# Performance work log

Hardware: AMD Instinct MI355X
Metric: run time of the kernel (lower is better)

The kernel has to match this reference:

```python
import jax, jax.numpy as jnp
import numpy as np

N = 100000      # nodes
D = 64          # raw node feature dim
E = 3200000     # edges
G = 128         # graphs in batch
RANK = 50
OVER = 10       # randomized-SVD oversampling
NPOW = 4        # subspace (power) iterations
ALPHA = 0.85    # pagerank alpha
HID = 32
NCLS = 696
F = 21 * D      # concat of [x] + 4 hop-1 + 16 hop-2 propagated tensors


def setup_inputs() -> dict:
    key = jax.random.key(0)
    ks = jax.random.split(key, 8)
    x = jax.random.normal(ks[0], (N, D), jnp.float32)
    rows = jax.random.randint(ks[1], (E,), 0, N, jnp.int32)
    cols = jax.random.randint(ks[2], (E,), 0, N, jnp.int32)
    graph_ids = jnp.sort(jax.random.randint(ks[3], (N,), 0, G, jnp.int32))
    w = jax.random.normal(ks[4], (F, 64), jnp.float32) / np.float32(np.sqrt(F))
    W1 = jax.random.normal(ks[5], (64, HID), jnp.float32) / np.float32(8.0)
    b1 = jnp.zeros((HID,), jnp.float32)
    W2 = jax.random.normal(ks[6], (HID, NCLS), jnp.float32) / np.float32(np.sqrt(HID))
    return dict(x=x, rows=rows, cols=cols, graph_ids=graph_ids, num_graphs=G,
                w=w, W1=W1, b1=b1, W2=W2)


def _prop_ops(X, rows, cols, deg, n):
    """Apply the 4 sparse operators to X. A[r,c]=1 per edge (rows[k], cols[k])."""
    ax = jax.ops.segment_sum(X[cols], rows, num_segments=n)          # A @ X
    t = ax / jnp.where(deg > 0, deg, 1.0)[:, None]                   # D^{-1} A @ X (transition)
    pr = ALPHA * t + ((1.0 - ALPHA) / n) * ax                        # pagerank-style operator
    dw = ax / (deg + 1e-5)[:, None]                                  # deepwalk: diag(1/(deg+eps)) A
    return [ax, t, pr, dw]


def _propagated(x, rows, cols):
    n = x.shape[0]
    deg = jax.ops.segment_sum(jnp.ones(rows.shape, x.dtype), rows, num_segments=n)
    h1 = _prop_ops(x, rows, cols, deg, n)                            # 4 tensors, hop 1
    h2 = [t2 for t1 in h1 for t2 in _prop_ops(t1, rows, cols, deg, n)]  # 16 tensors, hop 2
    return jnp.concatenate([x] + h1 + h2, axis=-1)                   # [n, 21*D]


def _rsvd(h, rank, key):
    """Deterministic randomized SVD (Halko et al.), QR-stabilized power iterations."""
    k = rank + OVER
    omega = jax.random.normal(key, (h.shape[1], k), h.dtype)
    Q = jnp.linalg.qr(h @ omega)[0]                                  # [n, k]
    for _ in range(NPOW):
        Q = jnp.linalg.qr(h.T @ Q)[0]
        Q = jnp.linalg.qr(h @ Q)[0]
    B = Q.T @ h                                                      # [k, F]
    ub, s, vt = jnp.linalg.svd(B, full_matrices=False)
    return (Q @ ub)[:, :rank], s[:rank], vt[:rank]


def reference(x, rows, cols, graph_ids, num_graphs, w, W1, b1, W2):
    h = _propagated(x, rows, cols)                                   # [n, F]
    u, s, vt = _rsvd(h, RANK, jax.random.key(42))
    us = u * s                                                       # [n, rank]
    term = us @ (vt @ w)                                             # [n, 64]
    hid = jax.nn.leaky_relu(term @ W1 + b1)                          # Dense + leaky_relu
    out_nodes = hid @ W2                                             # [n, num_classes]
    # pooling_adj.T.normalize_right(): each node belongs to exactly one graph,
    # so the column sums are 1 and this is a per-graph segment sum.
    return jax.ops.segment_sum(out_nodes, graph_ids, num_segments=num_graphs)
```

## Files before the change

### kernel.cpp

```cpp
#include <hip/hip_runtime.h>

#define NN   100000
#define DD   64
#define EE   3200000
#define GG   128
#define FF   1344
#define KK   60
#define RK   50
#define HIDN 32
#define NCL  696
#define BSPLIT 128
#define GSL  64
#define PN   40


typedef short short8 __attribute__((ext_vector_type(8)));
typedef float f32x4 __attribute__((ext_vector_type(4)));

__device__ __forceinline__ unsigned short f2bf(float x){
  unsigned u = __float_as_uint(x);
  unsigned r = u + 0x7fffu + ((u>>16)&1u);
  return (unsigned short)(r>>16);
}
__device__ __forceinline__ float bf2f(unsigned short h){
  return __uint_as_float(((unsigned)h)<<16);
}

__device__ __forceinline__ unsigned rotl32(unsigned x, unsigned r){ return (x<<r)|(x>>(32u-r)); }

__device__ __forceinline__ void threefry(unsigned& x0, unsigned& x1){
  const unsigned ks0 = 0u, ks1 = 42u, ks2 = 0x1BD11BDAu ^ 0u ^ 42u;
  unsigned ks[3] = {ks0, ks1, ks2};
  const unsigned rotA[4] = {13u,15u,26u,6u};
  const unsigned rotB[4] = {17u,29u,16u,24u};
  x0 += ks0; x1 += ks1;
  #pragma unroll
  for (int i = 0; i < 5; ++i){
    #pragma unroll
    for (int j = 0; j < 4; ++j){
      unsigned r = (i & 1) ? rotB[j] : rotA[j];
      x0 += x1; x1 = rotl32(x1, r); x1 ^= x0;
    }
    x0 += ks[(i+1)%3]; x1 += ks[(i+2)%3] + (unsigned)(i+1);
  }
}

__device__ __forceinline__ float bits_to_normal(unsigned bits){
  unsigned mant = bits >> 9;
  float f; { unsigned fb = 0x3f800000u | mant; f = __uint_as_float(fb); }
  f -= 1.0f;
  const float lo = -0.99999994f;
  float u = fmaf(f, 2.0f, lo);
  u = fmaxf(lo, u);
  float w = -log1pf(-u*u);
  float p;
  if (w < 5.0f){
    w -= 2.5f;
    p = 2.81022636e-08f;
    p = fmaf(p, w, 3.43273939e-07f);
    p = fmaf(p, w, -3.5233877e-06f);
    p = fmaf(p, w, -4.39150654e-06f);
    p = fmaf(p, w, 0.00021858087f);
    p = fmaf(p, w, -0.00125372503f);
    p = fmaf(p, w, -0.00417768164f);
    p = fmaf(p, w, 0.246640727f);
    p = fmaf(p, w, 1.50140941f);
  } else {
    w = sqrtf(w) - 3.0f;
    p = -0.000200214257f;
    p = fmaf(p, w, 0.000100950558f);
    p = fmaf(p, w, 0.00134934322f);
    p = fmaf(p, w, -0.00367342844f);
    p = fmaf(p, w, 0.00573950773f);
    p = fmaf(p, w, -0.0076224613f);
    p = fmaf(p, w, 0.00943887047f);
    p = fmaf(p, w, 1.00167406f);
    p = fmaf(p, w, 2.83297682f);
  }
  return 1.41421356f * (p * u);
}

__global__ void k_omega(float* __restrict__ om){
  int i = blockIdx.x*blockDim.x + threadIdx.x;
  if (i >= FF*KK) return;
  unsigned x0 = 0u, x1 = (unsigned)i;
  threefry(x0, x1);
  om[i] = bits_to_normal(x0 ^ x1);
}

__global__ void k_count(const int* __restrict__ rows, int* __restrict__ cnt){
  int e = blockIdx.x*blockDim.x + threadIdx.x;
  if (e < EE) atomicAdd(&cnt[rows[e]], 1);
}

__global__ __launch_bounds__(1024) void k_scan1(const int* __restrict__ cnt,
    int* __restrict__ incl, int* __restrict__ bsums){
  __shared__ int buf[1024];
  int i = blockIdx.x*1024 + threadIdx.x;
  int v = (i < NN) ? cnt[i] : 0;
  buf[threadIdx.x] = v; __syncthreads();
  for (int ofs = 1; ofs < 1024; ofs <<= 1){
    int add = (threadIdx.x >= (unsigned)ofs) ? buf[threadIdx.x - ofs] : 0;
    __syncthreads();
    buf[threadIdx.x] += add;
    __syncthreads();
  }
  if (i < NN) incl[i] = buf[threadIdx.x];
  if (threadIdx.x == 1023) bsums[blockIdx.x] = buf[1023];
}

__global__ void k_scan2(int* __restrict__ bsums, int nb){
  if (threadIdx.x == 0){
    int run = 0;
    for (int i = 0; i < nb; ++i){ int v = bsums[i]; bsums[i] = run; run += v; }
  }
}

__global__ void k_scan3(const int* __restrict__ cnt, const int* __restrict__ bsums,
                        int* __restrict__ rowptr){
  int i = blockIdx.x*blockDim.x + threadIdx.x;
  if (i >= NN) return;
  int incl = rowptr[i];
  int ex = incl - cnt[i] + bsums[i >> 10];
  rowptr[i] = ex;
  if (i == NN-1) rowptr[NN] = ex + cnt[i];
}

__global__ void k_scatter(const int* __restrict__ rows, const int* __restrict__ cols,
                          const int* __restrict__ rowptr, int* __restrict__ tmpc,
                          int* __restrict__ csr){
  int e = blockIdx.x*blockDim.x + threadIdx.x;
  if (e >= EE) return;
  int r = rows[e];
  int p = atomicAdd(&tmpc[r], 1);
  csr[rowptr[r] + p] = cols[e];
}

__global__ void k_degr(const int* __restrict__ cnt, float* __restrict__ r1, float* __restrict__ r2){
  int i = blockIdx.x*blockDim.x + threadIdx.x;
  if (i >= NN) return;
  int d = cnt[i];
  float fd = (float)d;
  r1[i] = (d > 0) ? 1.0f/fd : 1.0f;
  r2[i] = 1.0f/(fd + 1e-5f);
}

__global__ void k_xcvt(const float* __restrict__ x,
                       unsigned short* __restrict__ xh, unsigned short* __restrict__ xl){
  int gid = blockIdx.x*blockDim.x + threadIdx.x;
  if (gid >= NN*64) return;
  float v = x[gid];
  unsigned short h = f2bf(v);
  xh[gid] = h;
  xl[gid] = f2bf(v - bf2f(h));
}

__global__ __launch_bounds__(256) void k_hop1(const float* __restrict__ x,
    const int* __restrict__ rp, const int* __restrict__ cc, float* __restrict__ ax,
    unsigned short* __restrict__ axh, unsigned short* __restrict__ axl){
  int n = blockIdx.x*4 + (threadIdx.x >> 6);
  int lane = threadIdx.x & 63;
  if (n >= NN) return;
  int s = rp[n], e = rp[n+1];
  float acc = 0.f;
  int idx = s;
  for (; idx + 8 <= e; idx += 8){
    int c0 = cc[idx], c1 = cc[idx+1], c2 = cc[idx+2], c3 = cc[idx+3];
    int c4 = cc[idx+4], c5 = cc[idx+5], c6 = cc[idx+6], c7 = cc[idx+7];
    float v0 = x[(size_t)c0*64 + lane];
    float v1 = x[(size_t)c1*64 + lane];
    float v2 = x[(size_t)c2*64 + lane];
    float v3 = x[(size_t)c3*64 + lane];
    float v4 = x[(size_t)c4*64 + lane];
    float v5 = x[(size_t)c5*64 + lane];
    float v6 = x[(size_t)c6*64 + lane];
    float v7 = x[(size_t)c7*64 + lane];
    acc += ((v0 + v1) + (v2 + v3)) + ((v4 + v5) + (v6 + v7));
  }
  for (; idx < e; ++idx) acc += x[(size_t)cc[idx]*64 + lane];
  size_t o = (size_t)n*64 + lane;
  ax[o] = acc;
  unsigned short h = f2bf(acc);
  axh[o] = h;
  axl[o] = f2bf(acc - bf2f(h));
}

__global__ __launch_bounds__(256) void k_hop2(const int* __restrict__ rp, const int* __restrict__ cc,
    const float* __restrict__ ax, const float* __restrict__ r1, const float* __restrict__ r2,
    unsigned short* __restrict__ s0h, unsigned short* __restrict__ s0l,
    unsigned short* __restrict__ s1h, unsigned short* __restrict__ s1l,
    unsigned short* __restrict__ s3h, unsigned short* __restrict__ s3l){
  int n = blockIdx.x*4 + (threadIdx.x >> 6);
  int lane = threadIdx.x & 63;
  if (n >= NN) return;
  int s = rp[n], e = rp[n+1];
  float v_s0 = 0.f, v_s1 = 0.f, v_s3 = 0.f;
  int idx = s;
  for (; idx + 8 <= e; idx += 8){
    int c0 = cc[idx], c1 = cc[idx+1], c2 = cc[idx+2], c3 = cc[idx+3];
    int c4 = cc[idx+4], c5 = cc[idx+5], c6 = cc[idx+6], c7 = cc[idx+7];
    float v0 = ax[(size_t)c0*64 + lane], a0 = r1[c0], b0 = r2[c0];
    float v1 = ax[(size_t)c1*64 + lane], a1 = r1[c1], b1 = r2[c1];
    float v2 = ax[(size_t)c2*64 + lane], a2 = r1[c2], b2 = r2[c2];
    float v3 = ax[(size_t)c3*64 + lane], a3 = r1[c3], b3 = r2[c3];
    float v4 = ax[(size_t)c4*64 + lane], a4 = r1[c4], b4 = r2[c4];
    float v5 = ax[(size_t)c5*64 + lane], a5 = r1[c5], b5 = r2[c5];
    float v6 = ax[(size_t)c6*64 + lane], a6 = r1[c6], b6 = r2[c6];
    float v7 = ax[(size_t)c7*64 + lane], a7 = r1[c7], b7 = r2[c7];
    v_s0 += ((v0 + v1) + (v2 + v3)) + ((v4 + v5) + (v6 + v7));
    v_s1 = fmaf(v0,a0,fmaf(v1,a1,fmaf(v2,a2,fmaf(v3,a3,v_s1))));
    v_s1 = fmaf(v4,a4,fmaf(v5,a5,fmaf(v6,a6,fmaf(v7,a7,v_s1))));
    v_s3 = fmaf(v0,b0,fmaf(v1,b1,fmaf(v2,b2,fmaf(v3,b3,v_s3))));
    v_s3 = fmaf(v4,b4,fmaf(v5,b5,fmaf(v6,b6,fmaf(v7,b7,v_s3))));
  }
  for (; idx < e; ++idx){
    int c = cc[idx];
    float v = ax[(size_t)c*64 + lane];
    v_s0 += v;
    v_s1 = fmaf(v, r1[c], v_s1);
    v_s3 = fmaf(v, r2[c], v_s3);
  }
  size_t o = (size_t)n*64 + lane;
  unsigned short h0 = f2bf(v_s0);
  s0h[o] = h0; s0l[o] = f2bf(v_s0 - bf2f(h0));
  unsigned short h1 = f2bf(v_s1);
  s1h[o] = h1; s1l[o] = f2bf(v_s1 - bf2f(h1));
  unsigned short h3 = f2bf(v_s3);
  s3h[o] = h3; s3l[o] = f2bf(v_s3 - bf2f(h3));
}

__global__ void k_beff(const float* __restrict__ B,
                       unsigned short* __restrict__ Beh, unsigned short* __restrict__ Bel){
  int gid = blockIdx.x*blockDim.x + threadIdx.x;
  if (gid >= 20*4096) return;
  int p = gid >> 12;
  int rem = gid & 4095;
  int c = rem >> 6, r = rem & 63;
  int t = p >> 2, j = p & 3;
  float val = 0.f;
  if (c < KK){
    if (t == 0)      val = (j == 0) ? B[(0*64 + r)*60 + c] : 0.f;
    else if (t == 1) val = B[((1+j)*64 + r)*60 + c];
    else if (t == 2) val = B[((5+j)*64 + r)*60 + c] + 1.5e-6f*B[((13+j)*64 + r)*60 + c];
    else if (t == 3) val = B[((9+j)*64 + r)*60 + c] + 0.85f  *B[((13+j)*64 + r)*60 + c];
    else             val = B[((17+j)*64 + r)*60 + c];
  }
  unsigned short h = f2bf(val);
  Beh[gid] = h;
  Bel[gid] = f2bf(val - bf2f(h));
}

__global__ __launch_bounds__(256) void k_beffT(const float* __restrict__ Z,
    const float* __restrict__ Rtot,
    unsigned short* __restrict__ Beh, unsigned short* __restrict__ Bel){
  __shared__ float Br[64][61];
  __shared__ float Rt[60][64];
  int p = blockIdx.x;
  int t2 = p >> 2, j = p & 3;
  int tid = threadIdx.x;
  if (t2 == 0 && j != 0){
    for (int o = tid; o < 4096; o += 256){ Beh[(size_t)p*4096 + o] = 0; Bel[(size_t)p*4096 + o] = 0; }
    return;
  }
  for (int i = tid; i < 3840; i += 256){
    int r = i >> 6, c = i & 63;
    if (c < 60) Rt[r][c] = Rtot[r*60 + c];
  }
  for (int o = tid; o < 64*60; o += 256){
    int r = o / 60, k = o - (o/60)*60;
    float v;
    if (t2 == 0)      v = Z[(0*64 + r)*60 + k];
    else if (t2 == 1) v = Z[((1+j)*64 + r)*60 + k];
    else if (t2 == 2) v = Z[((5+j)*64 + r)*60 + k] + 1.5e-6f*Z[((13+j)*64 + r)*60 + k];
    else if (t2 == 3) v = Z[((9+j)*64 + r)*60 + k] + 0.85f  *Z[((13+j)*64 + r)*60 + k];
    else              v = Z[((17+j)*64 + r)*60 + k];
    Br[r][k] = v;
  }
  __syncthreads();
  for (int o = tid; o < 4096; o += 256){
    int c = o >> 6, r = o & 63;
    float s = 0.f;
    if (c < KK){
      #pragma unroll 10
      for (int kp = 0; kp < 60; ++kp) s = fmaf(Br[r][kp], Rt[kp][c], s);
    }
    unsigned short h = f2bf(s);
    Beh[(size_t)p*4096 + o] = h;
    Bel[(size_t)p*4096 + o] = f2bf(s - bf2f(h));
  }
}

__device__ __forceinline__ void fma44(const float4 a, const float4 b, float (&acc)[4][4]){
  acc[0][0] = fmaf(a.x,b.x,acc[0][0]); acc[0][1] = fmaf(a.x,b.y,acc[0][1]);
  acc[0][2] = fmaf(a.x,b.z,acc[0][2]); acc[0][3] = fmaf(a.x,b.w,acc[0][3]);
  acc[1][0] = fmaf(a.y,b.x,acc[1][0]); acc[1][1] = fmaf(a.y,b.y,acc[1][1]);
  acc[1][2] = fmaf(a.y,b.z,acc[1][2]); acc[1][3] = fmaf(a.y,b.w,acc[1][3]);
  acc[2][0] = fmaf(a.z,b.x,acc[2][0]); acc[2][1] = fmaf(a.z,b.y,acc[2][1]);
  acc[2][2] = fmaf(a.z,b.z,acc[2][2]); acc[2][3] = fmaf(a.z,b.w,acc[2][3]);
  acc[3][0] = fmaf(a.w,b.x,acc[3][0]); acc[3][1] = fmaf(a.w,b.y,acc[3][1]);
  acc[3][2] = fmaf(a.w,b.z,acc[3][2]); acc[3][3] = fmaf(a.w,b.w,acc[3][3]);
}

__global__ __launch_bounds__(256) void k_fwd(
    const unsigned short* __restrict__ xh, const unsigned short* __restrict__ xl,
    const unsigned short* __restrict__ axh, const unsigned short* __restrict__ axl,
    const unsigned short* __restrict__ s0h, const unsigned short* __restrict__ s0l,
    const unsigned short* __restrict__ s1h, const unsigned short* __restrict__ s1l,
    const unsigned short* __restrict__ s3h, const unsigned short* __restrict__ s3l,
    const unsigned short* __restrict__ Beh, const unsigned short* __restrict__ Bel,
    const float* __restrict__ r1, const float* __restrict__ r2,
    float* __restrict__ Y, float* __restrict__ Cpart){
  __shared__ __align__(16) unsigned short AB[4*64*72];
  __shared__ float cS[4][64];
  unsigned short* Ah = AB;
  unsigned short* Al = AB + 64*72;
  unsigned short* Bh = AB + 2*64*72;
  unsigned short* Bl = AB + 3*64*72;
  float* As2 = (float*)AB;
  const unsigned short* Tsh[5] = {xh, axh, s0h, s1h, s3h};
  const unsigned short* Tsl[5] = {xl, axl, s0l, s1l, s3l};
  int n0 = blockIdx.x*64;
  int tid = threadIdx.x;
  int lane = tid & 63, wid = tid >> 6;
  int rowb = (wid & 1)*32, colb = (wid >> 1)*32;
  int l15 = lane & 15, l4 = lane >> 4;

  if (tid < 64){
    int gn = n0 + tid;
    float r1v = 0.f, r2v = 0.f, one = 0.f;
    if (gn < NN){ r1v = r1[gn]; r2v = r2[gn]; one = 1.f; }
    cS[0][tid] = one;
    cS[1][tid] = r1v;
    cS[2][tid] = fmaf(0.85f, r1v, 1.5e-6f*one);
    cS[3][tid] = r2v;
  }

  f32x4 master[2][2] = {};
  int curt = -1;
  for (int plin = 0; plin < 17; ++plin){
    int t  = (plin == 0) ? 0 : (((plin-1) >> 2) + 1);
    int jj = (plin == 0) ? 0 : ((plin-1) & 3);
    int p  = (plin == 0) ? 0 : (plin + 3);
    if (t != curt){
      __syncthreads();
      const unsigned short* Th = Tsh[t];
      const unsigned short* Tl = Tsl[t];
      #pragma unroll
      for (int l = 0; l < 2; ++l){
        int li = tid + l*256;
        int n = li >> 3, f8 = (li & 7)*8;
        int gn = n0 + n;
        uint4 hv = make_uint4(0,0,0,0), lv = make_uint4(0,0,0,0);
        if (gn < NN){
          hv = *(const uint4*)(Th + (size_t)gn*64 + f8);
          lv = *(const uint4*)(Tl + (size_t)gn*64 + f8);
        }
        *(uint4*)(Ah + n*72 + f8) = hv;
        *(uint4*)(Al + n*72 + f8) = lv;
      }
      curt = t;
    }
    __syncthreads();
    #pragma unroll
    for (int l = 0; l < 2; ++l){
      int li = tid + l*256;
      int c = li >> 3, k8 = (li & 7)*8;
      uint4 hv = *(const uint4*)(Beh + (size_t)p*4096 + c*64 + k8);
      uint4 lv = *(const uint4*)(Bel + (size_t)p*4096 + c*64 + k8);
      *(uint4*)(Bh + c*72 + k8) = hv;
      *(uint4*)(Bl + c*72 + k8) = lv;
    }
    __syncthreads();

    float cvv[2][4];
    #pragma unroll
    for (int rg = 0; rg < 2; ++rg)
      #pragma unroll
      for (int r = 0; r < 4; ++r)
        cvv[rg][r] = cS[jj][rowb + rg*16 + l4*4 + r];

    f32x4 part[2][2] = {};
    #pragma unroll
    for (int s = 0; s < 2; ++s){
      int kc = s*32 + l4*8;
      short8 a0h = *(const short8*)(Ah + (rowb      + l15)*72 + kc);
      short8 a1h = *(const short8*)(Ah + (rowb + 16 + l15)*72 + kc);
      short8 a0l = *(const short8*)(Al + (rowb      + l15)*72 + kc);
      short8 a1l = *(const short8*)(Al + (rowb + 16 + l15)*72 + kc);
      #pragma unroll
      for (int cg = 0; cg < 2; ++cg){
        short8 bh = *(const short8*)(Bh + (colb + cg*16 + l15)*72 + kc);
        short8 bl = *(const short8*)(Bl + (colb + cg*16 + l15)*72 + kc);
        part[0][cg] = __builtin_amdgcn_mfma_f32_16x16x32_bf16(a0h, bh, part[0][cg], 0, 0, 0);
        part[0][cg] = __builtin_amdgcn_mfma_f32_16x16x32_bf16(a0h, bl, part[0][cg], 0, 0, 0);
        part[0][cg] = __builtin_amdgcn_mfma_f32_16x16x32_bf16(a0l, bh, part[0][cg], 0, 0, 0);
        part[1][cg] = __builtin_amdgcn_mfma_f32_16x16x32_bf16(a1h, bh, part[1][cg], 0, 0, 0);
        part[1][cg] = __builtin_amdgcn_mfma_f32_16x16x32_bf16(a1h, bl, part[1][cg], 0, 0, 0);
        part[1][cg] = __builtin_amdgcn_mfma_f32_16x16x32_bf16(a1l, bh, part[1][cg], 0, 0, 0);
      }
    }
    #pragma unroll
    for (int rg = 0; rg < 2; ++rg)
      #pragma unroll
      for (int cg = 0; cg < 2; ++cg)
        #pragma unroll
        for (int r = 0; r < 4; ++r)
          master[rg][cg][r] = fmaf(cvv[rg][r], part[rg][cg][r], master[rg][cg][r]);
  }

  #pragma unroll
  for (int rg = 0; rg < 2; ++rg)
    #pragma unroll
    for (int cg = 0; cg < 2; ++cg)
      #pragma unroll
      for (int r = 0; r < 4; ++r){
        int n = rowb + rg*16 + l4*4 + r;
        int c = colb + cg*16 + l15;
        int gn = n0 + n;
        if (gn < NN && c < KK) Y[(size_t)gn*KK + c] = master[rg][cg][r];
      }

  __syncthreads();
  #pragma unroll
  for (int rg = 0; rg < 2; ++rg)
    #pragma unroll
    for (int cg = 0; cg < 2; ++cg)
      #pragma unroll
      for (int r = 0; r < 4; ++r){
        int n = rowb + rg*16 + l4*4 + r;
        int c = colb + cg*16 + l15;
        As2[n*68 + c] = master[rg][cg][r];
      }
  __syncthreads();
  {
    int tx = tid & 15, ty = tid >> 4;
    float g[4][4] = {};
    #pragma unroll 4
    for (int n = 0; n < 64; ++n){
      float4 a = *(const float4*)(As2 + n*68 + tx*4);
      float4 b = *(const float4*)(As2 + n*68 + ty*4);
      fma44(a, b, g);
    }
    float* slab = Cpart + (size_t)(blockIdx.x & (GSL-1))*3600;
    #pragma unroll
    for (int i = 0; i < 4; ++i){
      int r = tx*4 + i;
      #pragma unroll
      for (int j = 0; j < 4; ++j){
        int c = ty*4 + j;
        if (r < KK && c < KK) atomicAdd(&slab[r*KK + c], g[i][j]);
      }
    }
  }
}

__global__ __launch_bounds__(256) void k_bwd(
    const unsigned short* __restrict__ xh, const unsigned short* __restrict__ xl,
    const unsigned short* __restrict__ axh, const unsigned short* __restrict__ axl,
    const unsigned short* __restrict__ s0h, const unsigned short* __restrict__ s0l,
    const unsigned short* __restrict__ s1h, const unsigned short* __restrict__ s1l,
    const unsigned short* __restrict__ s3h, const unsigned short* __restrict__ s3l,
    const float* __restrict__ Qm, const float* __restrict__ r1, const float* __restrict__ r2,
    float* __restrict__ Ppart){
  const unsigned short* Th = (blockIdx.x==0)?xh:(blockIdx.x==1)?axh:(blockIdx.x==2)?s0h:(blockIdx.x==3)?s1h:s3h;
  const unsigned short* Tl = (blockIdx.x==0)?xl:(blockIdx.x==1)?axl:(blockIdx.x==2)?s0l:(blockIdx.x==3)?s1l:s3l;
  const bool isX = (blockIdx.x == 0);
  const int TT = (NN + 31)/32;
  int per = (TT + BSPLIT - 1)/BSPLIT;
  int t0 = blockIdx.y * per;
  int t1 = t0 + per; if (t1 > TT) t1 = TT;

  __shared__ __align__(16) unsigned short Ah[64*PN];
  __shared__ __align__(16) unsigned short Al[64*PN];
  __shared__ __align__(16) unsigned short Bh3[3*64*PN];
  __shared__ __align__(16) unsigned short Bl3[3*64*PN];

  int tid = threadIdx.x;
  int lane = tid & 63, wid = tid >> 6;
  int rowb = (wid & 1)*32, colb = (wid >> 1)*32;
  int l15 = lane & 15, l4 = lane >> 4;

  for (int o = tid; o < 3*64*PN; o += 256){ Bh3[o] = 0; Bl3[o] = 0; }

  f32x4 master[3][2][2] = {};

  for (int tl = t0; tl < t1; ++tl){
    int nb = tl*32;
    __syncthreads();
    {
      int n = tid >> 3, f8 = (tid & 7)*8;
      int gn = nb + n;
      uint4 hv = make_uint4(0,0,0,0), lv = make_uint4(0,0,0,0);
      if (gn < NN){
        hv = *(const uint4*)(Th + (size_t)gn*64 + f8);
        lv = *(const uint4*)(Tl + (size_t)gn*64 + f8);
      }
      const unsigned short* hp = (const unsigned short*)&hv;
      const unsigned short* lp = (const unsigned short*)&lv;
      #pragma unroll
      for (int i = 0; i < 8; ++i){
        Ah[(f8+i)*PN + n] = hp[i];
        Al[(f8+i)*PN + n] = lp[i];
      }
    }
    #pragma unroll
    for (int l = 0; l < 2; ++l){
      int li = tid + l*256;
      if (li < 480){
        int n = li/15, cq = (li - (li/15)*15)*4;
        int gn = nb + n;
        float4 v = make_float4(0.f,0.f,0.f,0.f);
        float cc0 = 0.f, cc1 = 0.f, cc3 = 0.f;
        if (gn < NN){
          v = *(const float4*)(Qm + (size_t)gn*KK + cq);
          cc0 = 1.f;
          cc1 = isX ? 0.f : r1[gn];
          cc3 = isX ? 0.f : r2[gn];
        }
        float vv[4] = {v.x, v.y, v.z, v.w};
        float cc[3] = {cc0, cc1, cc3};
        #pragma unroll
        for (int jj = 0; jj < 3; ++jj){
          #pragma unroll
          for (int i = 0; i < 4; ++i){
            float sv = cc[jj]*vv[i];
            unsigned short h = f2bf(sv);
            Bh3[jj*64*PN + (cq+i)*PN + n] = h;
            Bl3[jj*64*PN + (cq+i)*PN + n] = f2bf(sv - bf2f(h));
          }
        }
      }
    }
    __syncthreads();
    short8 a0h = *(const short8*)(Ah + (rowb      + l15)*PN + l4*8);
    short8 a1h = *(const short8*)(Ah + (rowb + 16 + l15)*PN + l4*8);
    short8 a0l = *(const short8*)(Al + (rowb      + l15)*PN + l4*8);
    short8 a1l = *(const short8*)(Al + (rowb + 16 + l15)*PN + l4*8);
    #pragma unroll
    for (int jj = 0; jj < 3; ++jj){
      #pragma unroll
      for (int cg = 0; cg < 2; ++cg){
        short8 bh = *(const short8*)(Bh3 + jj*64*PN + (colb + cg*16 + l15)*PN + l4*8);
        short8 bl = *(const short8*)(Bl3 + jj*64*PN + (colb + cg*16 + l15)*PN + l4*8);
        master[jj][0][cg] = __builtin_amdgcn_mfma_f32_16x16x32_bf16(a0h, bh, master[jj][0][cg], 0, 0, 0);
        master[jj][0][cg] = __builtin_amdgcn_mfma_f32_16x16x32_bf16(a0h, bl, master[jj][0][cg], 0, 0, 0);
        master[jj][0][cg] = __builtin_amdgcn_mfma_f32_16x16x32_bf16(a0l, bh, master[jj][0][cg], 0, 0, 0);
        master[jj][1][cg] = __builtin_amdgcn_mfma_f32_16x16x32_bf16(a1h, bh, master[jj][1][cg], 0, 0, 0);
        master[jj][1][cg] = __builtin_amdgcn_mfma_f32_16x16x32_bf16(a1h, bl, master[jj][1][cg], 0, 0, 0);
        master[jj][1][cg] = __builtin_amdgcn_mfma_f32_16x16x32_bf16(a1l, bh, master[jj][1][cg], 0, 0, 0);
      }
    }
  }

  float* dst = Ppart + (size_t)blockIdx.y * 76800;
  #pragma unroll
  for (int jj = 0; jj < 3; ++jj){
    int j = (jj == 2) ? 3 : jj;
    #pragma unroll
    for (int rg = 0; rg < 2; ++rg)
      #pragma unroll
      for (int cg = 0; cg < 2; ++cg)
        #pragma unroll
        for (int r = 0; r < 4; ++r){
          int f = rowb + rg*16 + l4*4 + r;
          int kcol = colb + cg*16 + l15;
          if (kcol < KK)
            dst[(size_t)((blockIdx.x*4 + j)*64 + f)*60 + kcol] = master[jj][rg][cg][r];
        }
  }
}

__global__ void k_zasm(const float* __restrict__ Ppart, float* __restrict__ Z){
  int gid = blockIdx.x*blockDim.x + threadIdx.x;
  if (gid >= FF*KK) return;
  int f = gid / 60, k = gid - (gid/60)*60;
  int b = f >> 6, fi = f & 63;
  auto raw = [&](int t, int j)->float{
    size_t e = (size_t)((t*4 + j)*64 + fi)*60 + k;
    float s = 0.f;
    for (int bb = 0; bb < BSPLIT; ++bb) s += Ppart[(size_t)bb*76800 + e];
    return s;
  };
  auto fetch = [&](int t, int j)->float{
    if (j == 2) return 0.85f*raw(t,1) + 1.5e-6f*raw(t,0);
    return raw(t,j);
  };
  float val;
  if (b == 0)      val = raw(0,0);
  else if (b < 5)  val = fetch(1, b-1);
  else if (b < 9)  val = fetch(2, b-5);
  else if (b < 13) val = fetch(3, b-9);
  else if (b < 17) val = 0.85f*fetch(3, b-13) + 1.5e-6f*fetch(2, b-13);
  else             val = fetch(4, b-17);
  Z[gid] = val;
}

__global__ __launch_bounds__(256) void k_syrkp(const float* __restrict__ X, int nrows,
                                               float* __restrict__ Cpart){
  const int TTs = (nrows + 15)/16;
  int per = (TTs + gridDim.x - 1)/gridDim.x;
  int t0 = blockIdx.x*per;
  int t1 = t0 + per; if (t1 > TTs) t1 = TTs;
  __shared__ float Xs[16][64];
  int tid = threadIdx.x;
  int tx = tid & 15, ty = tid >> 4;
  float acc[4][4] = {};
  for (int tl = t0; tl < t1; ++tl){
    int nbase = tl*16;
    if (tid < 240){
      int n = tid / 15, ci = tid - (tid/15)*15;
      float4 v = make_float4(0.f,0.f,0.f,0.f);
      int gn = nbase + n;
      if (gn < nrows) v = *(const float4*)(X + (size_t)gn*KK + ci*4);
      *(float4*)&Xs[n][ci*4] = v;
    } else {
      int n = tid - 240;
      Xs[n][60]=0.f; Xs[n][61]=0.f; Xs[n][62]=0.f; Xs[n][63]=0.f;
    }
    __syncthreads();
    #pragma unroll
    for (int n = 0; n < 16; ++n){
      float4 a = *(const float4*)&Xs[n][tx*4];
      float4 b = *(const float4*)&Xs[n][ty*4];
      fma44(a, b, acc);
    }
    __syncthreads();
  }
  float* dst = Cpart + (size_t)blockIdx.x*3600;
  #pragma unroll
  for (int i = 0; i < 4; ++i){
    int r = tx*4 + i;
    #pragma unroll
    for (int j = 0; j < 4; ++j){
      int c = ty*4 + j;
      if (r < KK && c < KK) dst[r*KK + c] = acc[i][j];
    }
  }
}

__global__ void k_cred(const float* __restrict__ Cpart, int nparts, float* __restrict__ Cm){
  int gid = blockIdx.x*blockDim.x + threadIdx.x;
  if (gid >= 3600) return;
  float s = 0.f;
  for (int b = 0; b < nparts; ++b) s += Cpart[(size_t)b*3600 + gid];
  Cm[gid] = s;
}

__global__ __launch_bounds__(256) void k_cholinv(const float* __restrict__ Cin,
                                                 float* __restrict__ Rinv){
  __shared__ float R[60][65];
  __shared__ float Ri[60][65];
  __shared__ float Tmp[30][33];
  __shared__ float ridge;
  int t = threadIdx.x;
  for (int i = t; i < 3840; i += 256){
    int r = i >> 6, c = i & 63;
    if (c < 60) R[r][c] = Cin[r*60 + c];
  }
  __syncthreads();
  if (t == 0){
    float tr = 0.f;
    for (int i = 0; i < 60; ++i) tr += R[i][i];
    ridge = 1e-7f*(tr/60.f) + 1e-30f;
  }
  __syncthreads();
  if (t < 60) R[t][t] += ridge;
  __syncthreads();
  for (int j = 0; j < 60; ++j){
    float d  = fmaxf(R[j][j], 1e-30f);
    float dp = (j > 0) ? fmaxf(R[j-1][j-1], 1e-30f) : 1.f;
    float inv = 1.0f / d;
    float rsp = (j > 0) ? (1.0f / sqrtf(dp)) : 1.f;
    int nrow = 59 - j;
    for (int task = t; task < (nrow+1)*64; task += 256){
      int rr = task >> 6, i2 = task & 63;
      if (rr < nrow){
        int k = j + 1 + rr;
        if (i2 >= k && i2 < 60) R[k][i2] -= R[j][k]*R[j][i2]*inv;
      } else {
        if (j > 0 && i2 >= j-1 && i2 < 60) R[j-1][i2] *= rsp;
      }
    }
    __syncthreads();
  }
  if (t == 0) R[59][59] = sqrtf(fmaxf(R[59][59], 1e-30f));
  __syncthreads();
  for (int i = t; i < 3840; i += 256){ int r = i >> 6, c = i & 63; Ri[r][c] = 0.f; }
  __syncthreads();
  if (t < 60){
    int c = t;
    int lo = (c < 30) ? 0 : 30;
    Ri[c][c] = 1.0f / R[c][c];
    for (int i = c-1; i >= lo; --i){
      float s = 0.f;
      for (int k = i+1; k <= c; ++k) s += R[i][k]*Ri[k][c];
      Ri[i][c] = -s / R[i][i];
    }
  }
  __syncthreads();
  for (int idx2 = t; idx2 < 960; idx2 += 256){
    int r = idx2 >> 5, c = idx2 & 31;
    if (c < 30){
      float s = 0.f;
      for (int k = 0; k <= c; ++k) s += R[r][30+k]*Ri[30+k][30+c];
      Tmp[r][c] = s;
    }
  }
  __syncthreads();
  for (int idx2 = t; idx2 < 960; idx2 += 256){
    int r = idx2 >> 5, c = idx2 & 31;
    if (c < 30){
      float s = 0.f;
      for (int k = r; k < 30; ++k) s += Ri[r][k]*Tmp[k][c];
      Ri[r][30+c] = -s;
    }
  }
  __syncthreads();
  for (int i = t; i < 3600; i += 256) Rinv[i] = Ri[i/60][i%60];
}

__global__ __launch_bounds__(256) void k_cholinv2(const float* __restrict__ Gin,
                                                  float* __restrict__ Rinv){
  __shared__ float G[60][65];
  __shared__ float RN[60][65];
  __shared__ float T1[60][65];
  __shared__ float G2[60][65];
  __shared__ float Tmp[30][33];
  __shared__ float ridge;
  int t = threadIdx.x;
  for (int i = t; i < 3840; i += 256){
    int r = i >> 6, c = i & 63;
    if (c < 60){ G[r][c] = Gin[r*60 + c]; RN[r][c] = Rinv[r*60 + c]; }
  }
  __syncthreads();
  for (int o = t; o < 3600; o += 256){
    int i = o/60, j = o - (o/60)*60;
    float s = 0.f;
    for (int k = 0; k <= j; ++k) s = fmaf(G[i][k], RN[k][j], s);
    T1[i][j] = s;
  }
  __syncthreads();
  for (int o = t; o < 3600; o += 256){
    int i = o/60, j = o - (o/60)*60;
    float s = 0.f;
    for (int k = 0; k <= i; ++k) s = fmaf(RN[k][i], T1[k][j], s);
    G2[i][j] = s;
  }
  __syncthreads();
  if (t == 0){
    float tr = 0.f;
    for (int i = 0; i < 60; ++i) tr += G2[i][i];
    ridge = 1e-7f*(tr/60.f) + 1e-30f;
  }
  __syncthreads();
  if (t < 60) G2[t][t] += ridge;
  __syncthreads();
  for (int j = 0; j < 60; ++j){
    float d  = fmaxf(G2[j][j], 1e-30f);
    float dp = (j > 0) ? fmaxf(G2[j-1][j-1], 1e-30f) : 1.f;
    float inv = 1.0f / d;
    float rsp = (j > 0) ? (1.0f / sqrtf(dp)) : 1.f;
    int nrow = 59 - j;
    for (int task = t; task < (nrow+1)*64; task += 256){
      int rr = task >> 6, i2 = task & 63;
      if (rr < nrow){
        int k = j + 1 + rr;
        if (i2 >= k && i2 < 60) G2[k][i2] -= G2[j][k]*G2[j][i2]*inv;
      } else {
        if (j > 0 && i2 >= j-1 && i2 < 60) G2[j-1][i2] *= rsp;
      }
    }
    __syncthreads();
  }
  if (t == 0) G2[59][59] = sqrtf(fmaxf(G2[59][59], 1e-30f));
  __syncthreads();
  for (int i = t; i < 3840; i += 256){ int r = i >> 6, c = i & 63; T1[r][c] = 0.f; }
  __syncthreads();
  if (t < 60){
    int c = t;
    int lo = (c < 30) ? 0 : 30;
    T1[c][c] = 1.0f / G2[c][c];
    for (int i = c-1; i >= lo; --i){
      float s = 0.f;
      for (int k = i+1; k <= c; ++k) s += G2[i][k]*T1[k][c];
      T1[i][c] = -s / G2[i][i];
    }
  }
  __syncthreads();
  for (int idx2 = t; idx2 < 960; idx2 += 256){
    int r = idx2 >> 5, c = idx2 & 31;
    if (c < 30){
      float s = 0.f;
      for (int k = 0; k <= c; ++k) s += G2[r][30+k]*T1[30+k][30+c];
      Tmp[r][c] = s;
    }
  }
  __syncthreads();
  for (int idx2 = t; idx2 < 960; idx2 += 256){
    int r = idx2 >> 5, c = idx2 & 31;
    if (c < 30){
      float s = 0.f;
      for (int k = r; k < 30; ++k) s += T1[r][k]*Tmp[k][c];
      T1[r][30+c] = -s;
    }
  }
  __syncthreads();
  for (int o = t; o < 3600; o += 256){
    int i = o/60, j = o - (o/60)*60;
    float s = 0.f;
    if (i <= j){
      for (int k = i; k <= j; ++k) s = fmaf(RN[i][k], T1[k][j], s);
    }
    Rinv[o] = s;
  }
}

__global__ __launch_bounds__(256) void k_applyR(const float* Yin,
    const float* __restrict__ Rinv, float* Xout, int nrows){
  __shared__ float Rs[3600];
  for (int i = threadIdx.x; i < 3600; i += 256) Rs[i] = Rinv[i];
  __syncthreads();
  int w = threadIdx.x >> 6, lane = threadIdx.x & 63;
  #pragma unroll
  for (int r = 0; r < 4; ++r){
    int n = blockIdx.x*16 + w*4 + r;
    if (n >= nrows) continue;
    const float* y = Yin + (size_t)n*KK;
    float accv = 0.f;
    #pragma unroll 10
    for (int k2 = 0; k2 < KK; ++k2) accv = fmaf(y[k2], Rs[k2*KK + lane], accv);
    if (lane < KK) Xout[(size_t)n*KK + lane] = accv;
  }
}

__global__ void k_wb(const float* __restrict__ Z, const float* __restrict__ w,
                     float* __restrict__ WB){
  int gid = blockIdx.x*blockDim.x + threadIdx.x;
  if (gid >= KK*64) return;
  int r = gid >> 6, d = gid & 63;
  float acc = 0.f;
  for (int f = 0; f < FF; ++f) acc = fmaf(Z[(size_t)f*KK + r], w[(size_t)f*64 + d], acc);
  WB[gid] = acc;
}

__global__ __launch_bounds__(512) void k_jacobi(const float* __restrict__ Min,
                                                float* __restrict__ U50){
  __shared__ float A[60][65];
  __shared__ float Vv[60][65];
  __shared__ float cs[32], sn[32];
  __shared__ int pp[32], qq[32];
  __shared__ float ev[64];
  __shared__ int idx[64];
  int t = threadIdx.x;
  for (int i = t; i < 3840; i += 512){
    int r = i >> 6, c = i & 63;
    if (c < 60){ A[r][c] = Min[r*60 + c]; Vv[r][c] = (r == c) ? 1.f : 0.f; }
  }
  __syncthreads();
  for (int sweep = 0; sweep < 3; ++sweep){
    for (int round = 0; round < 59; ++round){
      if (t < 30){
        int i = t, j2 = 59 - t;
        int p = (i == 0) ? 0 : ((i - 1 + round) % 59 + 1);
        int q = ((j2 - 1 + round) % 59 + 1);
        if (p > q){ int tv = p; p = q; q = tv; }
        pp[t] = p; qq[t] = q;
        float app = A[p][p], aqq = A[q][q], apq = A[p][q];
        float c, s;
        if (fabsf(apq) < 1e-36f){ c = 1.f; s = 0.f; }
        else {
          float tau = (aqq - app) / (2.f * apq);
          float tt = ((tau >= 0.f) ? 1.f : -1.f) / (fabsf(tau) + sqrtf(1.f + tau*tau));
          c = 1.f / sqrtf(1.f + tt*tt);
          s = tt * c;
        }
        cs[t] = c; sn[t] = s;
      }
      __syncthreads();
      for (int task = t; task < 1920; task += 512){
        int k = task >> 6, i = task & 63;
        if (i < 60){
          int p = pp[k], q = qq[k];
          float c = cs[k], s = sn[k];
          float aip = A[i][p], aiq = A[i][q];
          A[i][p] = c*aip - s*aiq;  A[i][q] = s*aip + c*aiq;
          float vip = Vv[i][p], viq = Vv[i][q];
          Vv[i][p] = c*vip - s*viq; Vv[i][q] = s*vip + c*viq;
        }
      }
      __syncthreads();
      for (int task = t; task < 1920; task += 512){
        int k = task >> 6, i = task & 63;
        if (i < 60){
          int p = pp[k], q = qq[k];
          float c = cs[k], s = sn[k];
          float api = A[p][i], aqi = A[q][i];
          A[p][i] = c*api - s*aqi;  A[q][i] = s*api + c*aqi;
        }
      }
      __syncthreads();
    }
  }
  if (t < 60) ev[t] = A[t][t];
  __syncthreads();
  if (t < 60){
    float mine = ev[t];
    int rank = 0;
    for (int j = 0; j < 60; ++j){
      float o = ev[j];
      if (o > mine || (o == mine && j < t)) ++rank;
    }
    if (rank < RK) idx[rank] = t;
  }
  __syncthreads();
  for (int i2 = t; i2 < 60*RK; i2 += 512){
    int r = i2 / RK, c = i2 - (i2/RK)*RK;
    U50[i2] = Vv[r][idx[c]];
  }
}

__global__ __launch_bounds__(256) void k_chain(const float* __restrict__ U50,
    const float* __restrict__ WB, const float* __restrict__ W1, float* __restrict__ TW1){
  __shared__ float Us[60][52];
  __shared__ float WBs[60][64];
  __shared__ float G[50][64];
  __shared__ float Ts[60][64];
  int t = threadIdx.x;
  for (int i = t; i < 60*RK; i += 256) Us[i/RK][i%RK] = U50[i];
  for (int i = t; i < 3840; i += 256) WBs[i>>6][i&63] = WB[i];
  __syncthreads();
  for (int o = t; o < RK*64; o += 256){
    int r = o >> 6, d = o & 63;
    float acc = 0.f;
    #pragma unroll 10
    for (int i = 0; i < KK; ++i) acc = fmaf(Us[i][r], WBs[i][d], acc);
    G[r][d] = acc;
  }
  __syncthreads();
  for (int o = t; o < KK*64; o += 256){
    int i = o >> 6, d = o & 63;
    float acc = 0.f;
    #pragma unroll 10
    for (int r = 0; r < RK; ++r) acc = fmaf(Us[i][r], G[r][d], acc);
    Ts[i][d] = acc;
  }
  __syncthreads();
  for (int o = t; o < KK*HIDN; o += 256){
    int i = o >> 5, j = o & 31;
    float acc = 0.f;
    #pragma unroll 8
    for (int d = 0; d < 64; ++d) acc = fmaf(Ts[i][d], W1[d*HIDN + j], acc);
    TW1[o] = acc;
  }
}

__global__ __launch_bounds__(256) void k_hid(const float* __restrict__ Q,
    const float* __restrict__ TW1, const float* __restrict__ b1, float* __restrict__ hid){
  __shared__ float Ts[KK*HIDN];
  __shared__ float bs[HIDN];
  for (int i = threadIdx.x; i < KK*HIDN; i += 256) Ts[i] = TW1[i];
  if (threadIdx.x < HIDN) bs[threadIdx.x] = b1[threadIdx.x];
  __syncthreads();
  int gid = blockIdx.x*256 + threadIdx.x;
  if (gid >= NN*HIDN) return;
  int n = gid >> 5, j = gid & 31;
  const float* q = Q + (size_t)n*KK;
  float a = bs[j];
  #pragma unroll 10
  for (int k2 = 0; k2 < KK; ++k2) a = fmaf(q[k2], Ts[k2*HIDN + j], a);
  hid[gid] = (a >= 0.f) ? a : 0.01f*a;
}

__global__ void k_gstart(const int* __restrict__ gids, int* __restrict__ gst){
  int g = blockIdx.x*blockDim.x + threadIdx.x;
  if (g > GG) return;
  if (g == GG){ gst[GG] = NN; return; }
  int lo = 0, hi = NN;
  while (lo < hi){ int mid = (lo + hi) >> 1; if (gids[mid] < g) lo = mid + 1; else hi = mid; }
  gst[g] = lo;
}

__global__ __launch_bounds__(256) void k_gpool(const float* __restrict__ hid,
    const int* __restrict__ gst, float* __restrict__ pooled){
  int g = blockIdx.x;
  __shared__ float part[8][32];
  int w = threadIdx.x >> 5, lane = threadIdx.x & 31;
  int s = gst[g], e = gst[g+1];
  float acc = 0.f;
  for (int n = s + w; n < e; n += 8)
    acc += hid[(size_t)n*HIDN + lane];
  part[w][lane] = acc;
  __syncthreads();
  if (w == 0){
    float v = 0.f;
    #pragma unroll
    for (int i = 0; i < 8; ++i) v += part[i][lane];
    pooled[g*HIDN + lane] = v;
  }
}

__global__ void k_out(const float* __restrict__ pooled, const float* __restrict__ W2,
                      float* __restrict__ out){
  int gid = blockIdx.x*blockDim.x + threadIdx.x;
  if (gid >= GG*NCL) return;
  int g = gid / NCL, c = gid - (gid/NCL)*NCL;
  const float* p = pooled + g*HIDN;
  float acc = 0.f;
  #pragma unroll
  for (int k = 0; k < HIDN; ++k) acc = fmaf(p[k], W2[(size_t)k*NCL + c], acc);
  out[gid] = acc;
}

extern "C" void kernel_launch(void* const* d_in, const int* in_sizes, int n_in,
                              void* d_out, int out_size, void* d_ws, size_t ws_size,
                              hipStream_t stream){
  (void)in_sizes; (void)n_in; (void)out_size;
  const float* x   = (const float*)d_in[0];
  const int*  rows = (const int*)d_in[1];
  const int*  cols = (const int*)d_in[2];
  const int*  gids = (const int*)d_in[3];
  const float* wM  = (const float*)d_in[5];
  const float* W1  = (const float*)d_in[6];
  const float* b1  = (const float*)d_in[7];
  const float* W2  = (const float*)d_in[8];
  float* out = (float*)d_out;

  char* base = (char*)d_ws;
  size_t off = 0;
  auto alloc = [&](size_t bytes)->char*{
    off = (off + 255) & ~(size_t)255;
    char* p = base + off; off += bytes; return p;
  };
  float* ax    = (float*)alloc((size_t)NN*64*4);
  unsigned short* xh  = (unsigned short*)alloc((size_t)NN*64*2);
  unsigned short* xl  = (unsigned short*)alloc((size_t)NN*64*2);
  unsigned short* axh = (unsigned short*)alloc((size_t)NN*64*2);
  unsigned short* axl = (unsigned short*)alloc((size_t)NN*64*2);
  unsigned short* s0h = (unsigned short*)alloc((size_t)NN*64*2);
  unsigned short* s0l = (unsigned short*)alloc((size_t)NN*64*2);
  unsigned short* s1h = (unsigned short*)alloc((size_t)NN*64*2);
  unsigned short* s1l = (unsigned short*)alloc((size_t)NN*64*2);
  unsigned short* s3h = (unsigned short*)alloc((size_t)NN*64*2);
  unsigned short* s3l = (unsigned short*)alloc((size_t)NN*64*2);
  float* Y     = (float*)alloc((size_t)NN*KK*4);
  int*   csr   = (int*)  alloc((size_t)EE*4);
  float* Ppart = (float*)alloc((size_t)BSPLIT*76800*4);
  unsigned short* Beh = (unsigned short*)alloc((size_t)20*4096*2);
  unsigned short* Bel = (unsigned short*)alloc((size_t)20*4096*2);
  float* Om    = (float*)alloc((size_t)FF*KK*4);
  float* Zf    = (float*)alloc((size_t)FF*KK*4);
  float* Cm    = (float*)alloc(3600*4);
  float* Rinv  = (float*)alloc(3600*4);
  float* Mm    = (float*)alloc(3600*4);
  float* U50   = (float*)alloc(60*RK*4);
  float* WB    = (float*)alloc(KK*64*4);
  float* TW1   = (float*)alloc(KK*HIDN*4);
  float* pooled= (float*)alloc((size_t)GG*HIDN*4);
  float* r1    = (float*)alloc((size_t)NN*4);
  float* r2    = (float*)alloc((size_t)NN*4);
  int* cnt     = (int*)alloc((size_t)NN*4);
  int* rowptr  = (int*)alloc((size_t)(NN+1)*4);
  int* tmpc    = (int*)alloc((size_t)NN*4);
  int* gst     = (int*)alloc((size_t)(GG+1)*4);
  int* bsums   = (int*)alloc(256*4);
  float* hid   = ax;
  float* Cpart = Ppart;
  if (off > ws_size) return;

  const int SCAN_B = (NN + 1023) / 1024;

  hipMemsetAsync(cnt, 0, (size_t)NN*4, stream);
  k_count<<<(EE+255)/256, 256, 0, stream>>>(rows, cnt);
  k_scan1<<<SCAN_B, 1024, 0, stream>>>(cnt, rowptr, bsums);
  k_scan2<<<1, 64, 0, stream>>>(bsums, SCAN_B);
  k_scan3<<<(NN+255)/256, 256, 0, stream>>>(cnt, bsums, rowptr);
  hipMemsetAsync(tmpc, 0, (size_t)NN*4, stream);
  k_scatter<<<(EE+255)/256, 256, 0, stream>>>(rows, cols, rowptr, tmpc, csr);
  k_degr<<<(NN+255)/256, 256, 0, stream>>>(cnt, r1, r2);

  k_xcvt<<<(NN*64+255)/256, 256, 0, stream>>>(x, xh, xl);
  k_hop1<<<(NN+3)/4, 256, 0, stream>>>(x, rowptr, csr, ax, axh, axl);
  k_hop2<<<(NN+3)/4, 256, 0, stream>>>(rowptr, csr, ax, r1, r2, s0h, s0l, s1h, s1l, s3h, s3l);

  k_omega<<<(FF*KK+255)/256, 256, 0, stream>>>(Om);

  auto fwdg = [&](){
    hipMemsetAsync(Cpart, 0, (size_t)GSL*3600*4, stream);
    k_fwd<<<(NN+63)/64, 256, 0, stream>>>(xh, xl, axh, axl, s0h, s0l, s1h, s1l, s3h, s3l,
                                          Beh, Bel, r1, r2, Y, Cpart);
  };
  auto bwd = [&](const float* Qbuf){
    k_bwd<<<dim3(5, BSPLIT), 256, 0, stream>>>(xh, xl, axh, axl, s0h, s0l, s1h, s1l, s3h, s3l,
                                               Qbuf, r1, r2, Ppart);
    k_zasm<<<(FF*KK+255)/256, 256, 0, stream>>>(Ppart, Zf);
  };

  k_beff<<<(20*4096+255)/256, 256, 0, stream>>>(Om, Beh, Bel);
  fwdg();

  for (int it = 0; it < 4; ++it){
    k_cred<<<15, 256, 0, stream>>>(Cpart, GSL, Cm);
    k_cholinv<<<1, 256, 0, stream>>>(Cm, Rinv);
    bwd(Y);
    k_syrkp<<<84, 256, 0, stream>>>(Zf, FF, Cpart);
    k_cred<<<15, 256, 0, stream>>>(Cpart, 84, Cm);
    k_cholinv2<<<1, 256, 0, stream>>>(Cm, Rinv);
    k_beffT<<<20, 256, 0, stream>>>(Zf, Rinv, Beh, Bel);
    fwdg();
  }

  k_cred<<<15, 256, 0, stream>>>(Cpart, GSL, Cm);
  k_cholinv<<<1, 256, 0, stream>>>(Cm, Rinv);
  k_applyR<<<(NN+15)/16, 256, 0, stream>>>(Y, Rinv, Y, NN);

  bwd(Y);
  k_syrkp<<<84, 256, 0, stream>>>(Zf, FF, Cpart);
  k_cred<<<15, 256, 0, stream>>>(Cpart, 84, Mm);
  k_wb<<<(KK*64+255)/256, 256, 0, stream>>>(Zf, wM, WB);

  k_jacobi<<<1, 512, 0, stream>>>(Mm, U50);
  k_chain<<<1, 256, 0, stream>>>(U50, WB, W1, TW1);

  k_hid<<<(NN*HIDN+255)/256, 256, 0, stream>>>(Y, TW1, b1, hid);
  k_gstart<<<1, 256, 0, stream>>>(gids, gst);
  k_gpool<<<GG, 256, 0, stream>>>(hid, gst, pooled);
  k_out<<<(GG*NCL+255)/256, 256, 0, stream>>>(pooled, W2, out);
}
```

Before: 4.257 ms.

## Precompute scaled bf16 hi/lo transposed Q once per backward pass

Adds a k_qcvt kernel that scales Q by 1, r1 and r2, splits it into bf16 hi/lo parts and writes it feature-major, once per backward pass. Before, each of the five k_bwd block columns redid this scaling, splitting and strided shared-memory transposition on every tile. k_bwd now just copies contiguous 16-byte chunks into shared memory, and BSPLIT drops from 128 to 96. The cost is an extra launch and roughly 77 MB of extra traffic per iteration. The converted Q is stored in memory that aliases the dead ax and csr buffers, so this depends on the allocation order staying as is.

```diff
diff --git a/kernel.cpp b/kernel.cpp
--- a/kernel.cpp
+++ b/kernel.cpp
@@ -9,7 +9,7 @@
 #define RK   50
 #define HIDN 32
 #define NCL  696
-#define BSPLIT 128
+#define BSPLIT 96
 #define GSL  64
 #define PN   40
 
@@ -290,6 +290,39 @@
   }
 }
 
+__global__ __launch_bounds__(256) void k_qcvt(const float* __restrict__ Q,
+    const float* __restrict__ r1, const float* __restrict__ r2,
+    unsigned short* __restrict__ Qjh, unsigned short* __restrict__ Qjl){
+  __shared__ float Qs[64][65];
+  __shared__ float c1s[64], c3s[64];
+  int n0 = blockIdx.x*64;
+  int tid = threadIdx.x;
+  for (int i = tid; i < 64*60; i += 256){
+    int nl = i/60, k = i - (i/60)*60;
+    int gn = n0 + nl;
+    Qs[nl][k] = (gn < NN) ? Q[(size_t)gn*KK + k] : 0.f;
+  }
+  if (tid < 64){
+    int gn = n0 + tid;
+    c1s[tid] = (gn < NN) ? r1[gn] : 0.f;
+    c3s[tid] = (gn < NN) ? r2[gn] : 0.f;
+  }
+  __syncthreads();
+  for (int o = tid; o < 3*64*64; o += 256){
+    int nl = o & 63;
+    int jk = o >> 6;
+    int gn = n0 + nl;
+    if (gn >= NN) continue;
+    int j = jk >> 6, k = jk & 63;
+    float v = (k < KK) ? Qs[nl][k] : 0.f;
+    float c = (j == 0) ? 1.f : ((j == 1) ? c1s[nl] : c3s[nl]);
+    float sv = c * v;
+    unsigned short h = f2bf(sv);
+    Qjh[(size_t)jk*NN + gn] = h;
+    Qjl[(size_t)jk*NN + gn] = f2bf(sv - bf2f(h));
+  }
+}
+
 __device__ __forceinline__ void fma44(const float4 a, const float4 b, float (&acc)[4][4]){
   acc[0][0] = fmaf(a.x,b.x,acc[0][0]); acc[0][1] = fmaf(a.x,b.y,acc[0][1]);
   acc[0][2] = fmaf(a.x,b.z,acc[0][2]); acc[0][3] = fmaf(a.x,b.w,acc[0][3]);
@@ -460,11 +493,10 @@
     const unsigned short* __restrict__ s0h, const unsigned short* __restrict__ s0l,
     const unsigned short* __restrict__ s1h, const unsigned short* __restrict__ s1l,
     const unsigned short* __restrict__ s3h, const unsigned short* __restrict__ s3l,
-    const float* __restrict__ Qm, const float* __restrict__ r1, const float* __restrict__ r2,
+    const unsigned short* __restrict__ Qjh, const unsigned short* __restrict__ Qjl,
     float* __restrict__ Ppart){
   const unsigned short* Th = (blockIdx.x==0)?xh:(blockIdx.x==1)?axh:(blockIdx.x==2)?s0h:(blockIdx.x==3)?s1h:s3h;
   const unsigned short* Tl = (blockIdx.x==0)?xl:(blockIdx.x==1)?axl:(blockIdx.x==2)?s0l:(blockIdx.x==3)?s1l:s3l;
-  const bool isX = (blockIdx.x == 0);
   const int TT = (NN + 31)/32;
   int per = (TT + BSPLIT - 1)/BSPLIT;
   int t0 = blockIdx.y * per;
@@ -479,8 +511,6 @@
   int lane = tid & 63, wid = tid >> 6;
   int rowb = (wid & 1)*32, colb = (wid >> 1)*32;
   int l15 = lane & 15, l4 = lane >> 4;
-
-  for (int o = tid; o < 3*64*PN; o += 256){ Bh3[o] = 0; Bl3[o] = 0; }
 
   f32x4 master[3][2][2] = {};
 
@@ -504,32 +534,13 @@
       }
     }
     #pragma unroll
-    for (int l = 0; l < 2; ++l){
-      int li = tid + l*256;
-      if (li < 480){
-        int n = li/15, cq = (li - (li/15)*15)*4;
-        int gn = nb + n;
-        float4 v = make_float4(0.f,0.f,0.f,0.f);
-        float cc0 = 0.f, cc1 = 0.f, cc3 = 0.f;
-        if (gn < NN){
-          v = *(const float4*)(Qm + (size_t)gn*KK + cq);
-          cc0 = 1.f;
-          cc1 = isX ? 0.f : r1[gn];
-          cc3 = isX ? 0.f : r2[gn];
-        }
-        float vv[4] = {v.x, v.y, v.z, v.w};
-        float cc[3] = {cc0, cc1, cc3};
-        #pragma unroll
-        for (int jj = 0; jj < 3; ++jj){
-          #pragma unroll
-          for (int i = 0; i < 4; ++i){
-            float sv = cc[jj]*vv[i];
-            unsigned short h = f2bf(sv);
-            Bh3[jj*64*PN + (cq+i)*PN + n] = h;
-            Bl3[jj*64*PN + (cq+i)*PN + n] = f2bf(sv - bf2f(h));
-          }
-        }
-      }
+    for (int u = 0; u < 3; ++u){
+      int l = tid + u*256;
+      int row = l >> 2, ch = (l & 3)*8;
+      uint4 hv = *(const uint4*)(Qjh + (size_t)row*NN + nb + ch);
+      uint4 lv = *(const uint4*)(Qjl + (size_t)row*NN + nb + ch);
+      *(uint4*)(Bh3 + row*PN + ch) = hv;
+      *(uint4*)(Bl3 + row*PN + ch) = lv;
     }
     __syncthreads();
     short8 a0h = *(const short8*)(Ah + (rowb      + l15)*PN + l4*8);
@@ -1032,6 +1043,8 @@
     char* p = base + off; off += bytes; return p;
   };
   float* ax    = (float*)alloc((size_t)NN*64*4);
+  int*   csr   = (int*)  alloc((size_t)EE*4);
+  unsigned short* Qjh = (unsigned short*)ax;
   unsigned short* xh  = (unsigned short*)alloc((size_t)NN*64*2);
   unsigned short* xl  = (unsigned short*)alloc((size_t)NN*64*2);
   unsigned short* axh = (unsigned short*)alloc((size_t)NN*64*2);
@@ -1043,7 +1056,7 @@
   unsigned short* s3h = (unsigned short*)alloc((size_t)NN*64*2);
   unsigned short* s3l = (unsigned short*)alloc((size_t)NN*64*2);
   float* Y     = (float*)alloc((size_t)NN*KK*4);
-  int*   csr   = (int*)  alloc((size_t)EE*4);
+  unsigned short* Qjl = (unsigned short*)alloc((size_t)3*64*NN*2);
   float* Ppart = (float*)alloc((size_t)BSPLIT*76800*4);
   unsigned short* Beh = (unsigned short*)alloc((size_t)20*4096*2);
   unsigned short* Bel = (unsigned short*)alloc((size_t)20*4096*2);
@@ -1063,7 +1076,7 @@
   int* tmpc    = (int*)alloc((size_t)NN*4);
   int* gst     = (int*)alloc((size_t)(GG+1)*4);
   int* bsums   = (int*)alloc(256*4);
-  float* hid   = ax;
+  float* hid   = (float*)Qjl;
   float* Cpart = Ppart;
   if (off > ws_size) return;
 
@@ -1090,8 +1103,9 @@
                                           Beh, Bel, r1, r2, Y, Cpart);
   };
   auto bwd = [&](const float* Qbuf){
+    k_qcvt<<<(NN+63)/64, 256, 0, stream>>>(Qbuf, r1, r2, Qjh, Qjl);
     k_bwd<<<dim3(5, BSPLIT), 256, 0, stream>>>(xh, xl, axh, axl, s0h, s0l, s1h, s1l, s3h, s3l,
-                                               Qbuf, r1, r2, Ppart);
+                                               Qjh, Qjl, Ppart);
     k_zasm<<<(FF*KK+255)/256, 256, 0, stream>>>(Ppart, Zf);
   };
 
```

After: 4.033 ms. 1.06x faster.
